# Performance work log

Hardware: AMD Instinct MI355X
Metric: run time of the kernel (lower is better)

The kernel has to match this reference:

```python
import jax, jax.numpy as jnp
import numpy as np

TOP_K = 2  # num_experts_per_tok


def setup_inputs() -> dict:
    key = jax.random.key(0)
    k1, k2, k3, k4, k5 = jax.random.split(key, 5)
    B, S, D, F, E = 2, 1024, 1024, 2048, 8
    return {
        "x": jax.random.normal(k1, (B, S, D), dtype=jnp.float32),
        "router_kernel_DE": jax.random.normal(k2, (D, E), dtype=jnp.float32) * 0.02,
        "kernel_gating_EDF": jax.random.normal(k3, (E, D, F), dtype=jnp.float32) * 0.02,
        "kernel_up_EDF": jax.random.normal(k4, (E, D, F), dtype=jnp.float32) * 0.02,
        "kernel_down_EFD": jax.random.normal(k5, (E, F, D), dtype=jnp.float32) * 0.02,
    }


def reference(x, router_kernel_DE, kernel_gating_EDF, kernel_up_EDF, kernel_down_EFD):
    E = router_kernel_DE.shape[-1]
    x = x.astype(jnp.float32)
    # --- Router ---
    logits_BSE = jnp.einsum('BSD,DE->BSE', x, router_kernel_DE)
    probs_BSE = jax.nn.softmax(logits_BSE.astype(jnp.float32), axis=-1)
    weights_BSK, indices_BSK = jax.lax.top_k(probs_BSE, TOP_K)
    norm_weights_BSK = jax.nn.softmax(weights_BSK, axis=-1)
    # scatter top-k weights into dense [B,S,E]
    one_hot_BSKE = jax.nn.one_hot(indices_BSK, num_classes=E, dtype=x.dtype)
    full_weights_BSE = jnp.sum(one_hot_BSKE * norm_weights_BSK[..., None], axis=2)
    # --- Dense-over-all-experts MoE forward ---
    gating_BSEF = jnp.einsum('BSD,EDF->BSEF', x, kernel_gating_EDF)
    act_BSEF = jax.nn.silu(gating_BSEF)
    up_BSEF = jnp.einsum('BSD,EDF->BSEF', x, kernel_up_EDF)
    fuse_BSEF = act_BSEF * up_BSEF
    down_BSED = jnp.einsum('BSEF,EFD->BSED', fuse_BSEF, kernel_down_EFD)
    out_BSD = jnp.einsum('BSED,BSE->BSD', down_BSED, full_weights_BSE)
    return out_BSD.astype(jnp.float32)
```

## Files before the change

### kernel.cpp

```cpp
#include <hip/hip_runtime.h>
#include <hip/hip_bf16.h>
#include <stdint.h>

#define T_TOK 2048
#define DIM 1024
#define FDIM 2048
#define NEXP 8
#define NSLOT 4096
#define MAXTILE 64

typedef short bf16x8 __attribute__((ext_vector_type(8)));
typedef unsigned short u16x8 __attribute__((ext_vector_type(8)));
typedef float f32x4 __attribute__((ext_vector_type(4)));

__device__ __forceinline__ unsigned short f2bf(float f) {
  union { float f; unsigned int u; } v; v.f = f;
  unsigned int r = v.u + 0x7FFFu + ((v.u >> 16) & 1u);
  return (unsigned short)(r >> 16);
}

__device__ __forceinline__ float bf2f(unsigned short x) {
  union { unsigned int u; float f; } v; v.u = ((unsigned int)x) << 16;
  return v.f;
}

__device__ __forceinline__ void gld_lds16(const void* g, void* l) {
  __builtin_amdgcn_global_load_lds(
      (const __attribute__((address_space(1))) unsigned int*)g,
      (__attribute__((address_space(3))) unsigned int*)l, 16, 0, 0);
}

__global__ void router_kernel(const float* __restrict__ x, const float* __restrict__ rk,
                              int* __restrict__ counts, int* __restrict__ tok_e,
                              float* __restrict__ tok_w) {
  int w = threadIdx.x >> 6, lane = threadIdx.x & 63;
  int t = blockIdx.x * 4 + w;
  float acc[NEXP];
#pragma unroll
  for (int e = 0; e < NEXP; ++e) acc[e] = 0.f;
  const float4* xr = (const float4*)(x + (size_t)t * DIM);
#pragma unroll
  for (int i = 0; i < 4; ++i) {
    float4 xv = xr[i * 64 + lane];
    int d0 = (i * 64 + lane) * 4;
#pragma unroll
    for (int j = 0; j < 4; ++j) {
      const float4* rr = (const float4*)(rk + (size_t)(d0 + j) * NEXP);
      float4 r0 = rr[0], r1 = rr[1];
      float xs = (j == 0) ? xv.x : (j == 1) ? xv.y : (j == 2) ? xv.z : xv.w;
      acc[0] += xs * r0.x; acc[1] += xs * r0.y; acc[2] += xs * r0.z; acc[3] += xs * r0.w;
      acc[4] += xs * r1.x; acc[5] += xs * r1.y; acc[6] += xs * r1.z; acc[7] += xs * r1.w;
    }
  }
#pragma unroll
  for (int off = 32; off > 0; off >>= 1) {
#pragma unroll
    for (int e = 0; e < NEXP; ++e) acc[e] += __shfl_xor(acc[e], off, 64);
  }
  if (lane == 0) {
    float m = acc[0];
    for (int e = 1; e < NEXP; ++e) m = fmaxf(m, acc[e]);
    float p[NEXP], s = 0.f;
    for (int e = 0; e < NEXP; ++e) { p[e] = expf(acc[e] - m); s += p[e]; }
    float inv = 1.f / s;
    for (int e = 0; e < NEXP; ++e) p[e] *= inv;
    int i1 = 0;
    for (int e = 1; e < NEXP; ++e) if (p[e] > p[i1]) i1 = e;
    int i2 = (i1 == 0) ? 1 : 0;
    for (int e = 0; e < NEXP; ++e) if (e != i1 && p[e] > p[i2]) i2 = e;
    float e1 = expf(p[i1]), e2 = expf(p[i2]);
    float winv = 1.f / (e1 + e2);
    tok_e[t * 2] = i1; tok_e[t * 2 + 1] = i2;
    tok_w[t * 2] = e1 * winv; tok_w[t * 2 + 1] = e2 * winv;
    atomicAdd(&counts[i1], 1); atomicAdd(&counts[i2], 1);
  }
}

__global__ void scan_kernel(const int* __restrict__ counts, int* __restrict__ offsets,
                            int* __restrict__ tile_e, int* __restrict__ tile_mt,
                            int* __restrict__ ntiles) {
  if (threadIdx.x == 0) {
    int s = 0, t = 0;
    for (int e = 0; e < NEXP; ++e) {
      offsets[e] = s; s += counts[e];
      int nt = (counts[e] + 127) >> 7;
      for (int m = 0; m < nt; ++m) { tile_e[t] = e; tile_mt[t] = m; ++t; }
    }
    ntiles[0] = t;
  }
}

__global__ void assign_kernel(const int* __restrict__ tok_e, const float* __restrict__ tok_w,
                              const int* __restrict__ offsets, int* __restrict__ cursor,
                              int* __restrict__ slot_token, float* __restrict__ slot_weight,
                              int* __restrict__ tok_slot) {
  int t = blockIdx.x * 256 + threadIdx.x;
  if (t >= T_TOK) return;
#pragma unroll
  for (int k = 0; k < 2; ++k) {
    int e = tok_e[t * 2 + k];
    int pos = atomicAdd(&cursor[e], 1);
    int slot = offsets[e] + pos;
    slot_token[slot] = t;
    slot_weight[slot] = tok_w[t * 2 + k];
    tok_slot[t * 2 + k] = slot;
  }
}

__global__ void cvt_x_kernel(const float* __restrict__ x, unsigned short* __restrict__ xb) {
  int i = blockIdx.x * 256 + threadIdx.x;
  const float4* p = (const float4*)x;
  float4 a = p[i * 2], b = p[i * 2 + 1];
  uint4 o;
  o.x = ((unsigned)f2bf(a.y) << 16) | f2bf(a.x);
  o.y = ((unsigned)f2bf(a.w) << 16) | f2bf(a.z);
  o.z = ((unsigned)f2bf(b.y) << 16) | f2bf(b.x);
  o.w = ((unsigned)f2bf(b.w) << 16) | f2bf(b.z);
  ((uint4*)xb)[i] = o;
}

__global__ void transpose_cvt_kernel(const float* __restrict__ in, unsigned short* __restrict__ out,
                                     int R, int C) {
  __shared__ float lds[64][65];
  int e = blockIdx.z;
  size_t base = (size_t)e * (size_t)R * (size_t)C;
  int rb = blockIdx.y * 64, cb = blockIdx.x * 64;
  int tid = threadIdx.x;
  int col4 = (tid & 15) * 4, row = tid >> 4;
#pragma unroll
  for (int it = 0; it < 4; ++it) {
    int r = row + it * 16;
    float4 v = *(const float4*)(in + base + (size_t)(rb + r) * C + cb + col4);
    lds[col4 + 0][r] = v.x; lds[col4 + 1][r] = v.y;
    lds[col4 + 2][r] = v.z; lds[col4 + 3][r] = v.w;
  }
  __syncthreads();
  int r2 = (tid & 31) * 2, c = tid >> 5;
#pragma unroll
  for (int it = 0; it < 8; ++it) {
    int cc = c + it * 8;
    unsigned v = ((unsigned)f2bf(lds[cc][r2 + 1]) << 16) | f2bf(lds[cc][r2]);
    *(unsigned*)(out + base + (size_t)(cb + cc) * R + rb + r2) = v;
  }
}


__global__ __launch_bounds__(256) void gemm_gateup(
    const unsigned short* __restrict__ xb, const unsigned short* __restrict__ wg,
    const unsigned short* __restrict__ wu, const int* __restrict__ counts,
    const int* __restrict__ offsets, const int* __restrict__ slot_token,
    const int* __restrict__ tile_e, const int* __restrict__ tile_mt,
    const int* __restrict__ ntiles, unsigned short* __restrict__ fuse) {
  int ys = blockIdx.y;
  if (ys >= ntiles[0]) return;
  int e = tile_e[ys], mt = tile_mt[ys];
  int cnt = counts[e];
  int off = offsets[e];
  int nt = blockIdx.x;
  __shared__ unsigned short Al[128 * 64];
  __shared__ unsigned short Bgl[64 * 64];
  __shared__ unsigned short Bul[64 * 64];
  int tid = threadIdx.x, w = tid >> 6, lane = tid & 63;
  int csrc = ((lane & 7) ^ (lane >> 3)) * 8;
  unsigned aoff[4];
  unsigned boff[2];
#pragma unroll
  for (int ii = 0; ii < 4; ++ii) {
    int r = (w * 4 + ii) * 8 + (lane >> 3);
    int row = mt * 128 + r;
    int tok = (row < cnt) ? slot_token[off + row] : 0;
    aoff[ii] = (unsigned)(tok * DIM + csrc);
  }
#pragma unroll
  for (int ii = 0; ii < 2; ++ii) {
    int r = (w * 2 + ii) * 8 + (lane >> 3);
    boff[ii] = (unsigned)((e * FDIM + nt * 64 + r) * DIM + csrc);
  }
  f32x4 accg[4][2] = {};
  f32x4 accu[4][2] = {};
  int wr = (w >> 1) * 64, wc = (w & 1) * 32;
  int swz = (lane & 7) << 3;
  int kof0 = ((lane >> 4) * 8) ^ swz;
  int kof1 = (32 + (lane >> 4) * 8) ^ swz;
  for (int k0 = 0; k0 < DIM; k0 += 64) {
#pragma unroll
    for (int ii = 0; ii < 4; ++ii)
      gld_lds16(xb + aoff[ii] + k0, &Al[(w * 4 + ii) * 512]);
#pragma unroll
    for (int ii = 0; ii < 2; ++ii) {
      gld_lds16(wg + boff[ii] + k0, &Bgl[(w * 2 + ii) * 512]);
      gld_lds16(wu + boff[ii] + k0, &Bul[(w * 2 + ii) * 512]);
    }
    __syncthreads();
#pragma unroll
    for (int kk = 0; kk < 2; ++kk) {
      int kof = kk ? kof1 : kof0;
      bf16x8 af[4], bg[2], bu[2];
#pragma unroll
      for (int q = 0; q < 4; ++q)
        af[q] = *(const bf16x8*)&Al[(wr + q * 16 + (lane & 15)) * 64 + kof];
#pragma unroll
      for (int q = 0; q < 2; ++q) {
        bg[q] = *(const bf16x8*)&Bgl[(wc + q * 16 + (lane & 15)) * 64 + kof];
        bu[q] = *(const bf16x8*)&Bul[(wc + q * 16 + (lane & 15)) * 64 + kof];
      }
#pragma unroll
      for (int m4 = 0; m4 < 4; ++m4) {
#pragma unroll
        for (int n4 = 0; n4 < 2; ++n4) {
          accg[m4][n4] = __builtin_amdgcn_mfma_f32_16x16x32_bf16(af[m4], bg[n4], accg[m4][n4], 0, 0, 0);
          accu[m4][n4] = __builtin_amdgcn_mfma_f32_16x16x32_bf16(af[m4], bu[n4], accu[m4][n4], 0, 0, 0);
        }
      }
    }
    __syncthreads();
  }
#pragma unroll
  for (int m4 = 0; m4 < 4; ++m4) {
#pragma unroll
    for (int n4 = 0; n4 < 2; ++n4) {
      f32x4 g = accg[m4][n4], u = accu[m4][n4];
#pragma unroll
      for (int j = 0; j < 4; ++j) {
        int r = wr + m4 * 16 + (lane >> 4) * 4 + j;
        int row = mt * 128 + r;
        if (row < cnt) {
          float gv = g[j];
          float val = gv / (1.f + expf(-gv)) * u[j];
          int f = nt * 64 + wc + n4 * 16 + (lane & 15);
          fuse[(size_t)(off + row) * FDIM + f] = f2bf(val);
        }
      }
    }
  }
}

__global__ __launch_bounds__(256) void gemm_down(
    const unsigned short* __restrict__ fuse, const unsigned short* __restrict__ wd,
    const int* __restrict__ counts, const int* __restrict__ offsets,
    const float* __restrict__ slot_weight, const int* __restrict__ tile_e,
    const int* __restrict__ tile_mt, const int* __restrict__ ntiles,
    unsigned short* __restrict__ part4) {
  int ys = blockIdx.y;
  if (ys >= ntiles[0]) return;
  int e = tile_e[ys], mt = tile_mt[ys];
  int cnt = counts[e];
  int off = offsets[e];
  int nt = blockIdx.x;
  int z = blockIdx.z;
  int kbase = z * (FDIM / 4);
  __shared__ unsigned short Al[128 * 64];
  __shared__ unsigned short Bl[128 * 64];
  int tid = threadIdx.x, w = tid >> 6, lane = tid & 63;
  int csrc = ((lane & 7) ^ (lane >> 3)) * 8;
  unsigned aoff[4];
  unsigned boff[4];
#pragma unroll
  for (int ii = 0; ii < 4; ++ii) {
    int r = (w * 4 + ii) * 8 + (lane >> 3);
    int row = mt * 128 + r;
    int grow = (row < cnt) ? (off + row) : off;
    aoff[ii] = (unsigned)(grow * FDIM + kbase + csrc);
    boff[ii] = (unsigned)((e * DIM + nt * 128 + r) * FDIM + kbase + csrc);
  }
  f32x4 acc[4][4] = {};
  int wr = (w >> 1) * 64, wc = (w & 1) * 64;
  int swz = (lane & 7) << 3;
  int kof0 = ((lane >> 4) * 8) ^ swz;
  int kof1 = (32 + (lane >> 4) * 8) ^ swz;
  for (int k0 = 0; k0 < FDIM / 4; k0 += 64) {
#pragma unroll
    for (int ii = 0; ii < 4; ++ii) {
      gld_lds16(fuse + aoff[ii] + k0, &Al[(w * 4 + ii) * 512]);
      gld_lds16(wd + boff[ii] + k0, &Bl[(w * 4 + ii) * 512]);
    }
    __syncthreads();
#pragma unroll
    for (int kk = 0; kk < 2; ++kk) {
      int kof = kk ? kof1 : kof0;
      bf16x8 af[4], bfr[4];
#pragma unroll
      for (int q = 0; q < 4; ++q) {
        af[q] = *(const bf16x8*)&Al[(wr + q * 16 + (lane & 15)) * 64 + kof];
        bfr[q] = *(const bf16x8*)&Bl[(wc + q * 16 + (lane & 15)) * 64 + kof];
      }
#pragma unroll
      for (int m4 = 0; m4 < 4; ++m4) {
#pragma unroll
        for (int n4 = 0; n4 < 4; ++n4) {
          acc[m4][n4] = __builtin_amdgcn_mfma_f32_16x16x32_bf16(af[m4], bfr[n4], acc[m4][n4], 0, 0, 0);
        }
      }
    }
    __syncthreads();
  }
#pragma unroll
  for (int m4 = 0; m4 < 4; ++m4) {
#pragma unroll
    for (int j = 0; j < 4; ++j) {
      int r = wr + m4 * 16 + (lane >> 4) * 4 + j;
      int row = mt * 128 + r;
      if (row < cnt) {
        float wgt = slot_weight[off + row];
#pragma unroll
        for (int n4 = 0; n4 < 4; ++n4) {
          int d = nt * 128 + wc + n4 * 16 + (lane & 15);
          part4[((size_t)z * NSLOT + off + row) * DIM + d] = f2bf(acc[m4][n4][j] * wgt);
        }
      }
    }
  }
}

__global__ void combine_kernel(const unsigned short* __restrict__ part4,
                               const int* __restrict__ tok_slot, float* __restrict__ out) {
  int i = blockIdx.x * 256 + threadIdx.x;
  int t = i >> 7;
  int c = i & 127;
  int s0 = tok_slot[t * 2], s1 = tok_slot[t * 2 + 1];
  const u16x8* base = (const u16x8*)part4;
  float o[8];
#pragma unroll
  for (int j = 0; j < 8; ++j) o[j] = 0.f;
#pragma unroll
  for (int z = 0; z < 4; ++z) {
    u16x8 a = base[((size_t)z * NSLOT + s0) * (DIM / 8) + c];
    u16x8 b = base[((size_t)z * NSLOT + s1) * (DIM / 8) + c];
#pragma unroll
    for (int j = 0; j < 8; ++j) o[j] += bf2f(a[j]) + bf2f(b[j]);
  }
  float4* dst = (float4*)(out + (size_t)t * DIM + c * 8);
  dst[0] = make_float4(o[0], o[1], o[2], o[3]);
  dst[1] = make_float4(o[4], o[5], o[6], o[7]);
}

extern "C" void kernel_launch(void* const* d_in, const int* in_sizes, int n_in,
                              void* d_out, int out_size, void* d_ws, size_t ws_size,
                              hipStream_t stream) {
  (void)in_sizes; (void)n_in; (void)out_size;
  const float* x    = (const float*)d_in[0];
  const float* rk   = (const float*)d_in[1];
  const float* wg_f = (const float*)d_in[2];
  const float* wu_f = (const float*)d_in[3];
  const float* wd_f = (const float*)d_in[4];
  float* out = (float*)d_out;

  char* ws = (char*)d_ws;
  size_t o_xb   = 0;
  size_t o_wg   = o_xb + (size_t)T_TOK * DIM * 2;
  size_t o_wu   = o_wg + (size_t)NEXP * FDIM * DIM * 2;
  size_t o_wd   = o_wu + (size_t)NEXP * FDIM * DIM * 2;
  size_t o_fuse = o_wd + (size_t)NEXP * DIM * FDIM * 2;
  size_t o_part = o_fuse + (size_t)NSLOT * FDIM * 2;
  size_t o_meta = o_part + (size_t)2 * NSLOT * DIM * 2;
  size_t o_counts = o_meta;
  size_t o_cursor = o_counts + 32;
  size_t o_offs   = o_cursor + 32;
  size_t o_tok_e  = o_offs + 32;
  size_t o_tok_w  = o_tok_e + (size_t)T_TOK * 2 * 4;
  size_t o_tok_s  = o_tok_w + (size_t)T_TOK * 2 * 4;
  size_t o_st     = o_tok_s + (size_t)T_TOK * 2 * 4;
  size_t o_sw     = o_st + (size_t)NSLOT * 4;
  size_t o_te     = o_sw + (size_t)NSLOT * 4;
  size_t o_tm     = o_te + MAXTILE * 4;
  size_t o_ntl    = o_tm + MAXTILE * 4;
  size_t need     = o_ntl + 32;
  if (ws_size < need) return;

  unsigned short* xb    = (unsigned short*)(ws + o_xb);
  unsigned short* wgt   = (unsigned short*)(ws + o_wg);
  unsigned short* wut   = (unsigned short*)(ws + o_wu);
  unsigned short* wdt   = (unsigned short*)(ws + o_wd);
  unsigned short* fuse  = (unsigned short*)(ws + o_fuse);
  unsigned short* part4 = (unsigned short*)(ws + o_wg);
  int* counts          = (int*)(ws + o_counts);
  int* cursor          = (int*)(ws + o_cursor);
  int* offsets         = (int*)(ws + o_offs);
  int* tok_e           = (int*)(ws + o_tok_e);
  float* tok_w         = (float*)(ws + o_tok_w);
  int* tok_slot        = (int*)(ws + o_tok_s);
  int* slot_token      = (int*)(ws + o_st);
  float* slot_weight   = (float*)(ws + o_sw);
  int* tile_e          = (int*)(ws + o_te);
  int* tile_mt         = (int*)(ws + o_tm);
  int* ntiles          = (int*)(ws + o_ntl);

  hipMemsetAsync(ws + o_counts, 0, 64, stream);
  router_kernel<<<T_TOK / 4, 256, 0, stream>>>(x, rk, counts, tok_e, tok_w);
  scan_kernel<<<1, 64, 0, stream>>>(counts, offsets, tile_e, tile_mt, ntiles);
  assign_kernel<<<T_TOK / 256, 256, 0, stream>>>(tok_e, tok_w, offsets, cursor,
                                                 slot_token, slot_weight, tok_slot);
  cvt_x_kernel<<<(T_TOK * DIM / 8) / 256, 256, 0, stream>>>(x, xb);
  transpose_cvt_kernel<<<dim3(FDIM / 64, DIM / 64, NEXP), 256, 0, stream>>>(wg_f, wgt, DIM, FDIM);
  transpose_cvt_kernel<<<dim3(FDIM / 64, DIM / 64, NEXP), 256, 0, stream>>>(wu_f, wut, DIM, FDIM);
  transpose_cvt_kernel<<<dim3(DIM / 64, FDIM / 64, NEXP), 256, 0, stream>>>(wd_f, wdt, FDIM, DIM);

  gemm_gateup<<<dim3(FDIM / 64, 40, 1), 256, 0, stream>>>(
      xb, wgt, wut, counts, offsets, slot_token, tile_e, tile_mt, ntiles, fuse);
  gemm_down<<<dim3(DIM / 128, 40, 4), 256, 0, stream>>>(
      fuse, wdt, counts, offsets, slot_weight, tile_e, tile_mt, ntiles, part4);
  combine_kernel<<<(T_TOK * DIM / 8) / 256, 256, 0, stream>>>(part4, tok_slot, out);
}
```

Baseline: 267.0 us.

## Fold small kernels: merge x conversion into router, drop scan, unify weight transposes

Converts x to bf16 inside the router kernel, removing the separate conversion kernel. Removes the scan kernel: assign computes expert offsets from counts inline, and the GEMMs decode their tile-to-expert mapping from counts on the fly. The three weight transpose-convert launches become one combined launch, which now writes 8-byte vector stores instead of 4-byte ones. Together these cut the number of launches and serial dependencies, at the cost of each GEMM block repeating a small loop over counts.

```diff
diff --git a/kernel.cpp b/kernel.cpp
--- a/kernel.cpp
+++ b/kernel.cpp
@@ -7,7 +7,6 @@
 #define FDIM 2048
 #define NEXP 8
 #define NSLOT 4096
-#define MAXTILE 64
 
 typedef short bf16x8 __attribute__((ext_vector_type(8)));
 typedef unsigned short u16x8 __attribute__((ext_vector_type(8)));
@@ -32,7 +31,7 @@
 
 __global__ void router_kernel(const float* __restrict__ x, const float* __restrict__ rk,
                               int* __restrict__ counts, int* __restrict__ tok_e,
-                              float* __restrict__ tok_w) {
+                              float* __restrict__ tok_w, unsigned short* __restrict__ xb) {
   int w = threadIdx.x >> 6, lane = threadIdx.x & 63;
   int t = blockIdx.x * 4 + w;
   float acc[NEXP];
@@ -42,6 +41,10 @@
 #pragma unroll
   for (int i = 0; i < 4; ++i) {
     float4 xv = xr[i * 64 + lane];
+    uint2 pk;
+    pk.x = ((unsigned)f2bf(xv.y) << 16) | f2bf(xv.x);
+    pk.y = ((unsigned)f2bf(xv.w) << 16) | f2bf(xv.z);
+    *(uint2*)(xb + (size_t)t * DIM + (i * 64 + lane) * 4) = pk;
     int d0 = (i * 64 + lane) * 4;
 #pragma unroll
     for (int j = 0; j < 4; ++j) {
@@ -76,22 +79,8 @@
   }
 }
 
-__global__ void scan_kernel(const int* __restrict__ counts, int* __restrict__ offsets,
-                            int* __restrict__ tile_e, int* __restrict__ tile_mt,
-                            int* __restrict__ ntiles) {
-  if (threadIdx.x == 0) {
-    int s = 0, t = 0;
-    for (int e = 0; e < NEXP; ++e) {
-      offsets[e] = s; s += counts[e];
-      int nt = (counts[e] + 127) >> 7;
-      for (int m = 0; m < nt; ++m) { tile_e[t] = e; tile_mt[t] = m; ++t; }
-    }
-    ntiles[0] = t;
-  }
-}
-
 __global__ void assign_kernel(const int* __restrict__ tok_e, const float* __restrict__ tok_w,
-                              const int* __restrict__ offsets, int* __restrict__ cursor,
+                              const int* __restrict__ counts, int* __restrict__ cursor,
                               int* __restrict__ slot_token, float* __restrict__ slot_weight,
                               int* __restrict__ tok_slot) {
   int t = blockIdx.x * 256 + threadIdx.x;
@@ -99,32 +88,38 @@
 #pragma unroll
   for (int k = 0; k < 2; ++k) {
     int e = tok_e[t * 2 + k];
+    int off = 0;
+#pragma unroll
+    for (int j = 0; j < NEXP; ++j) off += (j < e) ? counts[j] : 0;
     int pos = atomicAdd(&cursor[e], 1);
-    int slot = offsets[e] + pos;
+    int slot = off + pos;
     slot_token[slot] = t;
     slot_weight[slot] = tok_w[t * 2 + k];
     tok_slot[t * 2 + k] = slot;
   }
 }
 
-__global__ void cvt_x_kernel(const float* __restrict__ x, unsigned short* __restrict__ xb) {
-  int i = blockIdx.x * 256 + threadIdx.x;
-  const float4* p = (const float4*)x;
-  float4 a = p[i * 2], b = p[i * 2 + 1];
-  uint4 o;
-  o.x = ((unsigned)f2bf(a.y) << 16) | f2bf(a.x);
-  o.y = ((unsigned)f2bf(a.w) << 16) | f2bf(a.z);
-  o.z = ((unsigned)f2bf(b.y) << 16) | f2bf(b.x);
-  o.w = ((unsigned)f2bf(b.w) << 16) | f2bf(b.z);
-  ((uint4*)xb)[i] = o;
-}
-
-__global__ void transpose_cvt_kernel(const float* __restrict__ in, unsigned short* __restrict__ out,
-                                     int R, int C) {
+__global__ void transpose_all(const float* __restrict__ wg_f, const float* __restrict__ wu_f,
+                              const float* __restrict__ wd_f, unsigned short* __restrict__ wgt,
+                              unsigned short* __restrict__ wut, unsigned short* __restrict__ wdt) {
   __shared__ float lds[64][65];
-  int e = blockIdx.z;
+  int bid = blockIdx.x, e = blockIdx.y;
+  const float* in;
+  unsigned short* out;
+  int R, C, rb, cb;
+  if (bid < 1024) {
+    in = (bid < 512) ? wg_f : wu_f;
+    out = (bid < 512) ? wgt : wut;
+    int id = bid & 511;
+    R = DIM; C = FDIM;
+    cb = (id & 31) * 64; rb = (id >> 5) * 64;
+  } else {
+    in = wd_f; out = wdt;
+    int id = bid - 1024;
+    R = FDIM; C = DIM;
+    cb = (id & 15) * 64; rb = (id >> 4) * 64;
+  }
   size_t base = (size_t)e * (size_t)R * (size_t)C;
-  int rb = blockIdx.y * 64, cb = blockIdx.x * 64;
   int tid = threadIdx.x;
   int col4 = (tid & 15) * 4, row = tid >> 4;
 #pragma unroll
@@ -135,27 +130,35 @@
     lds[col4 + 2][r] = v.z; lds[col4 + 3][r] = v.w;
   }
   __syncthreads();
-  int r2 = (tid & 31) * 2, c = tid >> 5;
-#pragma unroll
-  for (int it = 0; it < 8; ++it) {
-    int cc = c + it * 8;
-    unsigned v = ((unsigned)f2bf(lds[cc][r2 + 1]) << 16) | f2bf(lds[cc][r2]);
-    *(unsigned*)(out + base + (size_t)(cb + cc) * R + rb + r2) = v;
-  }
-}
-
+  int r4 = (tid & 15) * 4, c = tid >> 4;
+#pragma unroll
+  for (int it = 0; it < 4; ++it) {
+    int cc = c + it * 16;
+    uint2 v;
+    v.x = ((unsigned)f2bf(lds[cc][r4 + 1]) << 16) | f2bf(lds[cc][r4]);
+    v.y = ((unsigned)f2bf(lds[cc][r4 + 3]) << 16) | f2bf(lds[cc][r4 + 2]);
+    *(uint2*)(out + base + (size_t)(cb + cc) * R + rb + r4) = v;
+  }
+}
+
+__device__ __forceinline__ bool tile_decode(const int* counts, int ys, int& e, int& mt,
+                                            int& off, int& cnt) {
+  mt = ys; off = 0;
+  for (e = 0; e < NEXP; ++e) {
+    cnt = counts[e];
+    int ntl = (cnt + 127) >> 7;
+    if (mt < ntl) return true;
+    mt -= ntl; off += cnt;
+  }
+  return false;
+}
 
 __global__ __launch_bounds__(256) void gemm_gateup(
     const unsigned short* __restrict__ xb, const unsigned short* __restrict__ wg,
     const unsigned short* __restrict__ wu, const int* __restrict__ counts,
-    const int* __restrict__ offsets, const int* __restrict__ slot_token,
-    const int* __restrict__ tile_e, const int* __restrict__ tile_mt,
-    const int* __restrict__ ntiles, unsigned short* __restrict__ fuse) {
-  int ys = blockIdx.y;
-  if (ys >= ntiles[0]) return;
-  int e = tile_e[ys], mt = tile_mt[ys];
-  int cnt = counts[e];
-  int off = offsets[e];
+    const int* __restrict__ slot_token, unsigned short* __restrict__ fuse) {
+  int e, mt, off, cnt;
+  if (!tile_decode(counts, blockIdx.y, e, mt, off, cnt)) return;
   int nt = blockIdx.x;
   __shared__ unsigned short Al[128 * 64];
   __shared__ unsigned short Bgl[64 * 64];
@@ -237,15 +240,10 @@
 
 __global__ __launch_bounds__(256) void gemm_down(
     const unsigned short* __restrict__ fuse, const unsigned short* __restrict__ wd,
-    const int* __restrict__ counts, const int* __restrict__ offsets,
-    const float* __restrict__ slot_weight, const int* __restrict__ tile_e,
-    const int* __restrict__ tile_mt, const int* __restrict__ ntiles,
+    const int* __restrict__ counts, const float* __restrict__ slot_weight,
     unsigned short* __restrict__ part4) {
-  int ys = blockIdx.y;
-  if (ys >= ntiles[0]) return;
-  int e = tile_e[ys], mt = tile_mt[ys];
-  int cnt = counts[e];
-  int off = offsets[e];
+  int e, mt, off, cnt;
+  if (!tile_decode(counts, blockIdx.y, e, mt, off, cnt)) return;
   int nt = blockIdx.x;
   int z = blockIdx.z;
   int kbase = z * (FDIM / 4);
@@ -351,20 +349,15 @@
   size_t o_wu   = o_wg + (size_t)NEXP * FDIM * DIM * 2;
   size_t o_wd   = o_wu + (size_t)NEXP * FDIM * DIM * 2;
   size_t o_fuse = o_wd + (size_t)NEXP * DIM * FDIM * 2;
-  size_t o_part = o_fuse + (size_t)NSLOT * FDIM * 2;
-  size_t o_meta = o_part + (size_t)2 * NSLOT * DIM * 2;
+  size_t o_meta = o_fuse + (size_t)NSLOT * FDIM * 2;
   size_t o_counts = o_meta;
   size_t o_cursor = o_counts + 32;
-  size_t o_offs   = o_cursor + 32;
-  size_t o_tok_e  = o_offs + 32;
+  size_t o_tok_e  = o_cursor + 32;
   size_t o_tok_w  = o_tok_e + (size_t)T_TOK * 2 * 4;
   size_t o_tok_s  = o_tok_w + (size_t)T_TOK * 2 * 4;
   size_t o_st     = o_tok_s + (size_t)T_TOK * 2 * 4;
   size_t o_sw     = o_st + (size_t)NSLOT * 4;
-  size_t o_te     = o_sw + (size_t)NSLOT * 4;
-  size_t o_tm     = o_te + MAXTILE * 4;
-  size_t o_ntl    = o_tm + MAXTILE * 4;
-  size_t need     = o_ntl + 32;
+  size_t need     = o_sw + (size_t)NSLOT * 4;
   if (ws_size < need) return;
 
   unsigned short* xb    = (unsigned short*)(ws + o_xb);
@@ -375,29 +368,20 @@
   unsigned short* part4 = (unsigned short*)(ws + o_wg);
   int* counts          = (int*)(ws + o_counts);
   int* cursor          = (int*)(ws + o_cursor);
-  int* offsets         = (int*)(ws + o_offs);
   int* tok_e           = (int*)(ws + o_tok_e);
   float* tok_w         = (float*)(ws + o_tok_w);
   int* tok_slot        = (int*)(ws + o_tok_s);
   int* slot_token      = (int*)(ws + o_st);
   float* slot_weight   = (float*)(ws + o_sw);
-  int* tile_e          = (int*)(ws + o_te);
-  int* tile_mt         = (int*)(ws + o_tm);
-  int* ntiles          = (int*)(ws + o_ntl);
 
   hipMemsetAsync(ws + o_counts, 0, 64, stream);
-  router_kernel<<<T_TOK / 4, 256, 0, stream>>>(x, rk, counts, tok_e, tok_w);
-  scan_kernel<<<1, 64, 0, stream>>>(counts, offsets, tile_e, tile_mt, ntiles);
-  assign_kernel<<<T_TOK / 256, 256, 0, stream>>>(tok_e, tok_w, offsets, cursor,
+  router_kernel<<<T_TOK / 4, 256, 0, stream>>>(x, rk, counts, tok_e, tok_w, xb);
+  assign_kernel<<<T_TOK / 256, 256, 0, stream>>>(tok_e, tok_w, counts, cursor,
                                                  slot_token, slot_weight, tok_slot);
-  cvt_x_kernel<<<(T_TOK * DIM / 8) / 256, 256, 0, stream>>>(x, xb);
-  transpose_cvt_kernel<<<dim3(FDIM / 64, DIM / 64, NEXP), 256, 0, stream>>>(wg_f, wgt, DIM, FDIM);
-  transpose_cvt_kernel<<<dim3(FDIM / 64, DIM / 64, NEXP), 256, 0, stream>>>(wu_f, wut, DIM, FDIM);
-  transpose_cvt_kernel<<<dim3(DIM / 64, FDIM / 64, NEXP), 256, 0, stream>>>(wd_f, wdt, FDIM, DIM);
-
-  gemm_gateup<<<dim3(FDIM / 64, 40, 1), 256, 0, stream>>>(
-      xb, wgt, wut, counts, offsets, slot_token, tile_e, tile_mt, ntiles, fuse);
-  gemm_down<<<dim3(DIM / 128, 40, 4), 256, 0, stream>>>(
-      fuse, wdt, counts, offsets, slot_weight, tile_e, tile_mt, ntiles, part4);
+  transpose_all<<<dim3(1536, NEXP), 256, 0, stream>>>(wg_f, wu_f, wd_f, wgt, wut, wdt);
+  gemm_gateup<<<dim3(FDIM / 64, 40, 1), 256, 0, stream>>>(xb, wgt, wut, counts,
+                                                          slot_token, fuse);
+  gemm_down<<<dim3(DIM / 128, 40, 4), 256, 0, stream>>>(fuse, wdt, counts,
+                                                        slot_weight, part4);
   combine_kernel<<<(T_TOK * DIM / 8) / 256, 256, 0, stream>>>(part4, tok_slot, out);
 }
```

Result: faster. 249.3 us (-6.6%).
